# Kernel optimization log

Measured on AMD Instinct MI355X. Metric: run time of the kernel, lower is better.

The kernel has to match this reference:

```python
import jax, jax.numpy as jnp
import numpy as np

B, S, C, V, LAT, NL = 256, 512, 256, 32, 256, 7
DILS = [1, 2, 4, 8, 16, 32, 64]
EPS = 1e-5


def setup_inputs() -> dict:
    key = jax.random.key(0)
    ks = jax.random.split(key, 24)
    s = 0.05
    inp = {
        "x": jax.random.randint(ks[0], (B, S), 0, V, dtype=jnp.int64 if jax.config.read("jax_enable_x64") else jnp.int32),
        "z": jax.random.normal(ks[1], (B, LAT), dtype=jnp.float32),
        "emb": jax.random.normal(ks[2], (V, C), dtype=jnp.float32) * s,
        "latent_W": jax.random.normal(ks[3], (LAT, C), dtype=jnp.float32) * s,
        "latent_b": jnp.zeros((C,), jnp.float32),
        "ln1_g": jnp.ones((NL, C), jnp.float32),
        "ln1_b": jnp.zeros((NL, C), jnp.float32),
        "w1": jax.random.normal(ks[4], (NL, C, C), jnp.float32) * s,
        "b1": jnp.zeros((NL, C), jnp.float32),
        "ln2_g": jnp.ones((NL, C), jnp.float32),
        "ln2_b": jnp.zeros((NL, C), jnp.float32),
        "wd": jax.random.normal(ks[5], (NL, 2, C, C), jnp.float32) * s,  # tap 0 = x[t-d], tap 1 = x[t]
        "bd": jnp.zeros((NL, C), jnp.float32),
        "ln3_g": jnp.ones((NL, C), jnp.float32),
        "ln3_b": jnp.zeros((NL, C), jnp.float32),
        "we": jax.random.normal(ks[6], (NL, C, C), jnp.float32) * s,
        "be": jnp.zeros((NL, C), jnp.float32),
        "wg": jax.random.normal(ks[7], (NL, C, C), jnp.float32) * s,
        "bg": jnp.zeros((NL, C), jnp.float32),
        "out_W": jax.random.normal(ks[8], (C, V), jnp.float32) * s,
        "out_b": jnp.zeros((V,), jnp.float32),
    }
    return inp


def _ln(h, g, b):
    mu = h.mean(-1, keepdims=True)
    var = jnp.mean((h - mu) ** 2, axis=-1, keepdims=True)
    return (h - mu) * jax.lax.rsqrt(var + EPS) * g + b


def _lrelu(h):
    return jnp.where(h >= 0, h, 0.01 * h)


def reference(x, z, emb, latent_W, latent_b, ln1_g, ln1_b, w1, b1,
              ln2_g, ln2_b, wd, bd, ln3_g, ln3_b, we, be, wg, bg,
              out_W, out_b):
    # channel-last layout [B, S, C] throughout (fuses away the torch transposes)
    h = emb[x] + (z @ latent_W + latent_b)[:, None, :]
    for i, d in enumerate(DILS):
        x_inp = h
        t = _lrelu(_ln(x_inp, ln1_g[i], ln1_b[i]))
        t = t @ w1[i] + b1[i]
        t = _lrelu(_ln(t, ln2_g[i], ln2_b[i]))
        # causal dilated conv, kernel=2: out[t] = W0*x[t-d] + W1*x[t]
        t_shift = jnp.pad(t, ((0, 0), (d, 0), (0, 0)))[:, :t.shape[1], :]
        t = t_shift @ wd[i, 0] + t @ wd[i, 1] + bd[i]
        t = _lrelu(_ln(t, ln3_g[i], ln3_b[i]))
        gated = (t @ we[i] + be[i]) * jax.nn.sigmoid(t @ wg[i] + bg[i])
        h = gated + x_inp
    logits = h @ out_W + out_b                      # [B, S, V]
    lp = jax.nn.log_softmax(logits, axis=-1)
    # gather log-prob of next token: lp[:, :-1, :] at x[:, 1:]
    return jnp.take_along_axis(lp[:, :-1, :], x[:, 1:, None], axis=2)[..., 0]
```

## Files before the change

### kernel.cpp

```cpp
#include <hip/hip_runtime.h>

typedef unsigned short u16;
typedef unsigned int   u32;
typedef __attribute__((ext_vector_type(8))) short short8;
typedef __attribute__((ext_vector_type(4))) float f32x4;

struct __align__(8) u16x4 { u16 x, y, z, w; };

#define NL 7
#define M_DIM 131072

__device__ __forceinline__ float b2f(u16 u) {
  union { float f; u32 i; } c; c.i = ((u32)u) << 16; return c.f;
}
__device__ __forceinline__ u16 f2b(float f) {
  union { float f; u32 i; } c; c.f = f;
  u32 r = c.i + 0x7FFFu + ((c.i >> 16) & 1u);
  return (u16)(r >> 16);
}
__device__ __forceinline__ float wave_sum(float v) {
  #pragma unroll
  for (int off = 1; off < 64; off <<= 1) v += __shfl_xor(v, off);
  return v;
}
__device__ __forceinline__ void gload16(const void* g, void* l) {
  __builtin_amdgcn_global_load_lds((const __attribute__((address_space(1))) void*)g,
                                   (__attribute__((address_space(3))) void*)l, 16, 0, 0);
}


__global__ __launch_bounds__(256) void conv_w1_k(const float* __restrict__ w1, u16* __restrict__ wT) {
  int idx = blockIdx.x * 256 + threadIdx.x;
  int i = idx >> 16, rem = idx & 65535;
  int n = rem >> 8, k = rem & 255;
  wT[idx] = f2b(w1[(i << 16) + (k << 8) + n]);
}

__global__ __launch_bounds__(256) void conv_wd_k(const float* __restrict__ wd, u16* __restrict__ wT) {
  int idx = blockIdx.x * 256 + threadIdx.x;
  int i = idx / 131072, rem = idx & 131071;
  int n = rem >> 9, k2 = rem & 511;
  int tap = k2 >> 8, k = k2 & 255;
  wT[idx] = f2b(wd[(((i * 2 + tap) << 8) + k) * 256 + n]);
}

__global__ __launch_bounds__(256) void conv_weg_k(const float* __restrict__ we, const float* __restrict__ wg,
                                                  u16* __restrict__ wT) {
  int idx = blockIdx.x * 256 + threadIdx.x;
  int i = idx / 131072, rem = idx & 131071;
  int src = rem >> 16, n = (rem >> 8) & 255, k = rem & 255;
  const float* W = src ? wg : we;
  wT[idx] = f2b(W[((i << 8) + k) * 256 + n]);
}

__global__ __launch_bounds__(256) void conv_wo_k(const float* __restrict__ outW, u16* __restrict__ wTo) {
  int idx = blockIdx.x * 256 + threadIdx.x;
  int v = idx >> 8, k = idx & 255;
  wTo[idx] = f2b(outW[k * 32 + v]);
}


__global__ __launch_bounds__(256) void zlat_k(const float* __restrict__ z, const float* __restrict__ W,
                                              const float* __restrict__ bias, float* __restrict__ zlat) {
  int b = blockIdx.x, c = threadIdx.x;
  float acc = bias[c];
  for (int l = 0; l < 256; ++l) acc += z[b * 256 + l] * W[l * 256 + c];
  zlat[b * 256 + c] = acc;
}


__device__ __forceinline__ void ln_lrelu4(float v0, float v1, float v2, float v3,
                                          const float* __restrict__ g, const float* __restrict__ b,
                                          int c, u16x4* out) {
  float s = wave_sum(v0 + v1 + v2 + v3);
  float q = wave_sum(v0 * v0 + v1 * v1 + v2 * v2 + v3 * v3);
  float mu = s * 0.00390625f;
  float var = q * 0.00390625f - mu * mu;
  float rs = rsqrtf(var + 1e-5f);
  float4 gv = *(const float4*)&g[c];
  float4 bv = *(const float4*)&b[c];
  float y0 = (v0 - mu) * rs * gv.x + bv.x; y0 = y0 >= 0.f ? y0 : 0.01f * y0;
  float y1 = (v1 - mu) * rs * gv.y + bv.y; y1 = y1 >= 0.f ? y1 : 0.01f * y1;
  float y2 = (v2 - mu) * rs * gv.z + bv.z; y2 = y2 >= 0.f ? y2 : 0.01f * y2;
  float y3 = (v3 - mu) * rs * gv.w + bv.w; y3 = y3 >= 0.f ? y3 : 0.01f * y3;
  out->x = f2b(y0); out->y = f2b(y1); out->z = f2b(y2); out->w = f2b(y3);
}


__global__ __launch_bounds__(256) void embed_ln_k(const int* __restrict__ x, const float* __restrict__ emb,
                                                  const float* __restrict__ zlat,
                                                  const float* __restrict__ g, const float* __restrict__ b,
                                                  u16* __restrict__ h, u16* __restrict__ tOut) {
  int wave = threadIdx.x >> 6, lane = threadIdx.x & 63;
  int r = blockIdx.x * 4 + wave;
  int c = lane * 4;
  int tok = x[r];
  int bi = r >> 9;
  float4 ev = *(const float4*)&emb[tok * 256 + c];
  float4 zv = *(const float4*)&zlat[bi * 256 + c];
  float v0 = ev.x + zv.x, v1 = ev.y + zv.y, v2 = ev.z + zv.z, v3 = ev.w + zv.w;
  u16x4 hb; hb.x = f2b(v0); hb.y = f2b(v1); hb.z = f2b(v2); hb.w = f2b(v3);
  *(u16x4*)&h[(long)r * 256 + c] = hb;
  u16x4 ov;
  ln_lrelu4(v0, v1, v2, v3, g, b, c, &ov);
  *(u16x4*)&tOut[(long)r * 256 + c] = ov;
}


__global__ __launch_bounds__(256) void gemm_ln_k(
    const u16* __restrict__ A, const u16* __restrict__ WT, int Ktot, int dil,
    const float* __restrict__ bias, const float* __restrict__ g, const float* __restrict__ b,
    u16* __restrict__ Out)
{
  __shared__ u16 lA[64 * 32];
  __shared__ u16 lB[256 * 32];
  __shared__ float pS[64][4], pQ[64][4];
  __shared__ float muA[64], rsA[64];
  const int tid = threadIdx.x;
  const int lane = tid & 63;
  const int wv = tid >> 6;
  const int wc = wv * 64;
  const int m0 = blockIdx.x * 64;
  const int rA = tid >> 2;
  const int cSw = ((((tid & 3) - ((tid >> 3) & 3)) & 3)) * 8;
  const int mm = m0 + rA;
  const int s1 = mm & 511;
  const bool fixBlk = (dil > 0) && ((m0 & 511) < dil);

  const int lr = lane & 15;
  const int quad = lane >> 4;
  const int sw = ((quad + ((lr >> 1) & 3)) & 3) * 8;

  f32x4 acc[4][4];
  #pragma unroll
  for (int i = 0; i < 4; ++i)
    #pragma unroll
    for (int j = 0; j < 4; ++j) {
      acc[i][j][0] = 0.f; acc[i][j][1] = 0.f; acc[i][j][2] = 0.f; acc[i][j][3] = 0.f;
    }

  const int nkt = Ktot >> 5;
  for (int kt = 0; kt < nkt; ++kt) {
    const int kk = (kt & 7) * 32;
    int r = mm;
    if (dil > 0 && kt < 8) r = (s1 >= dil) ? (mm - dil) : mm;
    gload16(A + (long)r * 256 + kk + cSw, &lA[tid * 8]);
    const u16* bSrc = WT + (long)rA * Ktot + kt * 32 + cSw;
    #pragma unroll
    for (int j = 0; j < 4; ++j)
      gload16(bSrc + (long)(64 * j) * Ktot, &lB[tid * 8 + j * 2048]);
    __syncthreads();

    if (fixBlk && kt < 8) {
      if (rA < dil) {
        uint4 zz; zz.x = 0; zz.y = 0; zz.z = 0; zz.w = 0;
        *(uint4*)&lA[rA * 32 + (tid & 3) * 8] = zz;
      }
      __syncthreads();
    }

    short8 af[4], bfr[4];
    #pragma unroll
    for (int mt = 0; mt < 4; ++mt)
      af[mt] = *(const short8*)&lA[(mt * 16 + lr) * 32 + sw];
    #pragma unroll
    for (int nt = 0; nt < 4; ++nt)
      bfr[nt] = *(const short8*)&lB[(wc + nt * 16 + lr) * 32 + sw];
    #pragma unroll
    for (int mt = 0; mt < 4; ++mt)
      #pragma unroll
      for (int nt = 0; nt < 4; ++nt)
        acc[mt][nt] = __builtin_amdgcn_mfma_f32_16x16x32_bf16(af[mt], bfr[nt], acc[mt][nt], 0, 0, 0);
    __syncthreads();
  }

  float biasv[4], gv[4], bv[4];
  #pragma unroll
  for (int nt = 0; nt < 4; ++nt) {
    int n = wc + nt * 16 + lr;
    biasv[nt] = bias[n]; gv[nt] = g[n]; bv[nt] = b[n];
  }
  #pragma unroll
  for (int mt = 0; mt < 4; ++mt)
    #pragma unroll
    for (int r = 0; r < 4; ++r) {
      float s = 0.f, q = 0.f;
      #pragma unroll
      for (int nt = 0; nt < 4; ++nt) {
        float v = acc[mt][nt][r] + biasv[nt];
        acc[mt][nt][r] = v;
        s += v; q += v * v;
      }
      #pragma unroll
      for (int off = 1; off < 16; off <<= 1) {
        s += __shfl_xor(s, off); q += __shfl_xor(q, off);
      }
      if (lr == 0) { pS[mt * 16 + quad * 4 + r][wv] = s; pQ[mt * 16 + quad * 4 + r][wv] = q; }
    }
  __syncthreads();
  if (tid < 64) {
    float S = pS[tid][0] + pS[tid][1] + pS[tid][2] + pS[tid][3];
    float Q = pQ[tid][0] + pQ[tid][1] + pQ[tid][2] + pQ[tid][3];
    float mu = S * 0.00390625f;
    float var = Q * 0.00390625f - mu * mu;
    muA[tid] = mu; rsA[tid] = rsqrtf(var + 1e-5f);
  }
  __syncthreads();
  #pragma unroll
  for (int mt = 0; mt < 4; ++mt)
    #pragma unroll
    for (int r = 0; r < 4; ++r) {
      int row = mt * 16 + quad * 4 + r;
      float mu = muA[row], rs = rsA[row];
      #pragma unroll
      for (int nt = 0; nt < 4; ++nt) {
        float y = (acc[mt][nt][r] - mu) * rs * gv[nt] + bv[nt];
        y = y >= 0.f ? y : 0.01f * y;
        Out[(long)(m0 + row) * 256 + wc + nt * 16 + lr] = f2b(y);
      }
    }
}


__global__ __launch_bounds__(256, 2) void gemm_gate_ln_k(
    const u16* __restrict__ P, const u16* __restrict__ WTe, const u16* __restrict__ WTg,
    const float* __restrict__ be, const float* __restrict__ bg,
    const float* __restrict__ g, const float* __restrict__ b,
    u16* __restrict__ h, u16* __restrict__ tOut, int doLN)
{
  __shared__ u16 lA[64 * 32];
  __shared__ u16 lBe[256 * 32];
  __shared__ u16 lBg[256 * 32];
  __shared__ float pS[64][4], pQ[64][4];
  __shared__ float muA[64], rsA[64];
  const int tid = threadIdx.x;
  const int lane = tid & 63;
  const int wv = tid >> 6;
  const int wc = wv * 64;
  const int m0 = blockIdx.x * 64;
  const int rA = tid >> 2;
  const int cSw = ((((tid & 3) - ((tid >> 3) & 3)) & 3)) * 8;

  const int lr = lane & 15;
  const int quad = lane >> 4;
  const int sw = ((quad + ((lr >> 1) & 3)) & 3) * 8;

  f32x4 accE[4][4], accG[4][4];
  #pragma unroll
  for (int i = 0; i < 4; ++i)
    #pragma unroll
    for (int j = 0; j < 4; ++j) {
      accE[i][j][0] = 0.f; accE[i][j][1] = 0.f; accE[i][j][2] = 0.f; accE[i][j][3] = 0.f;
      accG[i][j][0] = 0.f; accG[i][j][1] = 0.f; accG[i][j][2] = 0.f; accG[i][j][3] = 0.f;
    }

  for (int kt = 0; kt < 8; ++kt) {
    const int kk = kt * 32;
    gload16(P + (long)(m0 + rA) * 256 + kk + cSw, &lA[tid * 8]);
    const long bofs = (long)rA * 256 + kk + cSw;
    #pragma unroll
    for (int j = 0; j < 4; ++j) {
      gload16(WTe + bofs + (long)(64 * j) * 256, &lBe[tid * 8 + j * 2048]);
      gload16(WTg + bofs + (long)(64 * j) * 256, &lBg[tid * 8 + j * 2048]);
    }
    __syncthreads();

    short8 af[4], bfe[4], bfg[4];
    #pragma unroll
    for (int mt = 0; mt < 4; ++mt)
      af[mt] = *(const short8*)&lA[(mt * 16 + lr) * 32 + sw];
    #pragma unroll
    for (int nt = 0; nt < 4; ++nt) {
      bfe[nt] = *(const short8*)&lBe[(wc + nt * 16 + lr) * 32 + sw];
      bfg[nt] = *(const short8*)&lBg[(wc + nt * 16 + lr) * 32 + sw];
    }
    #pragma unroll
    for (int mt = 0; mt < 4; ++mt)
      #pragma unroll
      for (int nt = 0; nt < 4; ++nt) {
        accE[mt][nt] = __builtin_amdgcn_mfma_f32_16x16x32_bf16(af[mt], bfe[nt], accE[mt][nt], 0, 0, 0);
        accG[mt][nt] = __builtin_amdgcn_mfma_f32_16x16x32_bf16(af[mt], bfg[nt], accG[mt][nt], 0, 0, 0);
      }
    __syncthreads();
  }

  float bev[4], bgv[4];
  #pragma unroll
  for (int nt = 0; nt < 4; ++nt) {
    int n = wc + nt * 16 + lr;
    bev[nt] = be[n]; bgv[nt] = bg[n];
  }
  #pragma unroll
  for (int mt = 0; mt < 4; ++mt)
    #pragma unroll
    for (int r = 0; r < 4; ++r) {
      int row = mt * 16 + quad * 4 + r;
      long off = (long)(m0 + row) * 256;
      float s = 0.f, q = 0.f;
      #pragma unroll
      for (int nt = 0; nt < 4; ++nt) {
        int n = wc + nt * 16 + lr;
        float e = accE[mt][nt][r] + bev[nt];
        float gg = accG[mt][nt][r] + bgv[nt];
        float hv = b2f(h[off + n]);
        float hn = e * (1.f / (1.f + expf(-gg))) + hv;
        h[off + n] = f2b(hn);
        accE[mt][nt][r] = hn;
        s += hn; q += hn * hn;
      }
      #pragma unroll
      for (int off2 = 1; off2 < 16; off2 <<= 1) {
        s += __shfl_xor(s, off2); q += __shfl_xor(q, off2);
      }
      if (lr == 0) { pS[row][wv] = s; pQ[row][wv] = q; }
    }
  __syncthreads();
  if (tid < 64) {
    float S = pS[tid][0] + pS[tid][1] + pS[tid][2] + pS[tid][3];
    float Q = pQ[tid][0] + pQ[tid][1] + pQ[tid][2] + pQ[tid][3];
    float mu = S * 0.00390625f;
    float var = Q * 0.00390625f - mu * mu;
    muA[tid] = mu; rsA[tid] = rsqrtf(var + 1e-5f);
  }
  __syncthreads();
  if (doLN) {
    float gv[4], bv[4];
    #pragma unroll
    for (int nt = 0; nt < 4; ++nt) {
      int n = wc + nt * 16 + lr;
      gv[nt] = g[n]; bv[nt] = b[n];
    }
    #pragma unroll
    for (int mt = 0; mt < 4; ++mt)
      #pragma unroll
      for (int r = 0; r < 4; ++r) {
        int row = mt * 16 + quad * 4 + r;
        float mu = muA[row], rs = rsA[row];
        #pragma unroll
        for (int nt = 0; nt < 4; ++nt) {
          float y = (accE[mt][nt][r] - mu) * rs * gv[nt] + bv[nt];
          y = y >= 0.f ? y : 0.01f * y;
          tOut[(long)(m0 + row) * 256 + wc + nt * 16 + lr] = f2b(y);
        }
      }
  }
}


__global__ __launch_bounds__(256) void final_k(const u16* __restrict__ h, const u16* __restrict__ WTo,
                                               const float* __restrict__ outb, const int* __restrict__ x,
                                               float* __restrict__ out) {
  __shared__ u16 lW[32 * 264];
  const int tid = threadIdx.x;
  const int lane = tid & 63;
  const int wv = tid >> 6;
  const int mBase = blockIdx.x * 256 + wv * 64;

  #pragma unroll
  for (int j = 0; j < 4; ++j) {
    int chunk = tid + 256 * j;
    int v = chunk >> 5, k8 = chunk & 31;
    uint4 w4 = *(const uint4*)(WTo + v * 256 + k8 * 8);
    *(uint4*)&lW[v * 264 + k8 * 8] = w4;
  }
  __syncthreads();

  const int lq = (lane >> 4) * 8;
  const int lr = lane & 15;
  const int quad = lane >> 4;

  f32x4 acc[4][2];
  #pragma unroll
  for (int mt = 0; mt < 4; ++mt) {
    acc[mt][0][0] = 0.f; acc[mt][0][1] = 0.f; acc[mt][0][2] = 0.f; acc[mt][0][3] = 0.f;
    acc[mt][1][0] = 0.f; acc[mt][1][1] = 0.f; acc[mt][1][2] = 0.f; acc[mt][1][3] = 0.f;
  }

  for (int kt = 0; kt < 8; ++kt) {
    short8 bf0 = *(const short8*)&lW[lr * 264 + kt * 32 + lq];
    short8 bf1 = *(const short8*)&lW[(16 + lr) * 264 + kt * 32 + lq];
    #pragma unroll
    for (int mt = 0; mt < 4; ++mt) {
      short8 af = *(const short8*)(h + (long)(mBase + mt * 16 + lr) * 256 + kt * 32 + lq);
      acc[mt][0] = __builtin_amdgcn_mfma_f32_16x16x32_bf16(af, bf0, acc[mt][0], 0, 0, 0);
      acc[mt][1] = __builtin_amdgcn_mfma_f32_16x16x32_bf16(af, bf1, acc[mt][1], 0, 0, 0);
    }
  }

  float ob0 = outb[lr], ob1 = outb[16 + lr];
  #pragma unroll
  for (int mt = 0; mt < 4; ++mt)
    #pragma unroll
    for (int r = 0; r < 4; ++r) {
      int row = mBase + mt * 16 + quad * 4 + r;
      float lo = acc[mt][0][r] + ob0;
      float hi = acc[mt][1][r] + ob1;
      float mx = fmaxf(lo, hi);
      #pragma unroll
      for (int o = 1; o < 16; o <<= 1) mx = fmaxf(mx, __shfl_xor(mx, o));
      float se = expf(lo - mx) + expf(hi - mx);
      #pragma unroll
      for (int o = 1; o < 16; o <<= 1) se += __shfl_xor(se, o);
      int s = row & 511;
      int xa = (s == 511) ? row : (row + 1);
      int tok = x[xa];
      float lg = (tok < 16) ? lo : hi;
      float lp = lg - mx - logf(se);
      if (s != 511 && lr == (tok & 15))
        out[(row >> 9) * 511 + s] = lp;
    }
}


extern "C" void kernel_launch(void* const* d_in, const int* in_sizes, int n_in,
                              void* d_out, int out_size, void* d_ws, size_t ws_size,
                              hipStream_t stream) {
  const int*   x    = (const int*)d_in[0];
  const float* z    = (const float*)d_in[1];
  const float* emb  = (const float*)d_in[2];
  const float* latW = (const float*)d_in[3];
  const float* latb = (const float*)d_in[4];
  const float* ln1g = (const float*)d_in[5];
  const float* ln1b = (const float*)d_in[6];
  const float* w1   = (const float*)d_in[7];
  const float* b1   = (const float*)d_in[8];
  const float* ln2g = (const float*)d_in[9];
  const float* ln2b = (const float*)d_in[10];
  const float* wd   = (const float*)d_in[11];
  const float* bd   = (const float*)d_in[12];
  const float* ln3g = (const float*)d_in[13];
  const float* ln3b = (const float*)d_in[14];
  const float* we   = (const float*)d_in[15];
  const float* be   = (const float*)d_in[16];
  const float* wg   = (const float*)d_in[17];
  const float* bg   = (const float*)d_in[18];
  const float* outW = (const float*)d_in[19];
  const float* outb = (const float*)d_in[20];

  char* ws = (char*)d_ws;
  u16*   h    = (u16*)(ws + 0);
  u16*   bufA = (u16*)(ws + 67108864);
  u16*   bufB = (u16*)(ws + 134217728);
  float* zlat = (float*)(ws + 201326592);
  u16*   wT1  = (u16*)(ws + 201588736);
  u16*   wTd  = (u16*)(ws + 202506240);
  u16*   wTeg = (u16*)(ws + 204341248);
  u16*   wTo  = (u16*)(ws + 206176256);

  conv_w1_k <<<1792, 256, 0, stream>>>(w1, wT1);
  conv_wd_k <<<3584, 256, 0, stream>>>(wd, wTd);
  conv_weg_k<<<3584, 256, 0, stream>>>(we, wg, wTeg);
  conv_wo_k <<<32, 256, 0, stream>>>(outW, wTo);
  zlat_k    <<<256, 256, 0, stream>>>(z, latW, latb, zlat);
  embed_ln_k<<<M_DIM / 4, 256, 0, stream>>>(x, emb, zlat, ln1g, ln1b, h, bufA);

  u16* X = bufA;
  u16* Y = bufB;
  for (int i = 0; i < NL; ++i) {
    int d = 1 << i;
    int doLN = (i < NL - 1) ? 1 : 0;
    int ni = doLN ? (i + 1) : i;
    gemm_ln_k<<<M_DIM / 64, 256, 0, stream>>>(
        X, wT1 + i * 65536, 256, 0, b1 + i * 256, ln2g + i * 256, ln2b + i * 256, Y);
    gemm_ln_k<<<M_DIM / 64, 256, 0, stream>>>(
        Y, wTd + i * 131072, 512, d, bd + i * 256, ln3g + i * 256, ln3b + i * 256, X);
    gemm_gate_ln_k<<<M_DIM / 64, 256, 0, stream>>>(
        X, wTeg + i * 131072, wTeg + i * 131072 + 65536, be + i * 256, bg + i * 256,
        ln1g + ni * 256, ln1b + ni * 256, h, Y, doLN);
    u16* tmp = X; X = Y; Y = tmp;
  }

  final_k<<<M_DIM / 256, 256, 0, stream>>>(h, wTo, outb, x, (float*)d_out);
}
```

Baseline: 1.667 ms.

## Enlarge GEMM row tiles to 128 and split gate GEMM across more waves

The row tile of both GEMM+LayerNorm kernels doubles to 128 rows, with 8 waves (gemm_ln) or 16 waves (gate kernel) laid out as an M×N wave grid, so each weight tile loaded into LDS is reused by twice as many rows. In the gate kernel each wave now computes only the E or only the G accumulator. Sigmoid results pass between waves through an LDS exchange buffer stored as bf16, which halves per-wave register pressure but adds a barrier and rounds the gate to bf16. The dilation zero-fix condition is changed to apply only to blocks at sequence start.

```diff
diff --git a/kernel.cpp b/kernel.cpp
--- a/kernel.cpp
+++ b/kernel.cpp
@@ -107,26 +107,26 @@
 }
 
 
-__global__ __launch_bounds__(256) void gemm_ln_k(
+__global__ __launch_bounds__(512, 4) void gemm_ln_k(
     const u16* __restrict__ A, const u16* __restrict__ WT, int Ktot, int dil,
     const float* __restrict__ bias, const float* __restrict__ g, const float* __restrict__ b,
     u16* __restrict__ Out)
 {
-  __shared__ u16 lA[64 * 32];
+  __shared__ u16 lA[128 * 32];
   __shared__ u16 lB[256 * 32];
-  __shared__ float pS[64][4], pQ[64][4];
-  __shared__ float muA[64], rsA[64];
+  __shared__ float pS[128][4], pQ[128][4];
+  __shared__ float muA[128], rsA[128];
   const int tid = threadIdx.x;
   const int lane = tid & 63;
   const int wv = tid >> 6;
-  const int wc = wv * 64;
-  const int m0 = blockIdx.x * 64;
+  const int mw = wv >> 2;
+  const int nw = wv & 3;
+  const int m0 = blockIdx.x * 128;
   const int rA = tid >> 2;
   const int cSw = ((((tid & 3) - ((tid >> 3) & 3)) & 3)) * 8;
   const int mm = m0 + rA;
   const int s1 = mm & 511;
-  const bool fixBlk = (dil > 0) && ((m0 & 511) < dil);
-
+  const bool fixBlk = (dil > 0) && ((m0 & 511) == 0);
   const int lr = lane & 15;
   const int quad = lane >> 4;
   const int sw = ((quad + ((lr >> 1) & 3)) & 3) * 8;
@@ -145,10 +145,9 @@
     int r = mm;
     if (dil > 0 && kt < 8) r = (s1 >= dil) ? (mm - dil) : mm;
     gload16(A + (long)r * 256 + kk + cSw, &lA[tid * 8]);
-    const u16* bSrc = WT + (long)rA * Ktot + kt * 32 + cSw;
-    #pragma unroll
-    for (int j = 0; j < 4; ++j)
-      gload16(bSrc + (long)(64 * j) * Ktot, &lB[tid * 8 + j * 2048]);
+    const u16* bSrc = WT + kt * 32 + cSw;
+    gload16(bSrc + (long)rA * Ktot,         &lB[tid * 8]);
+    gload16(bSrc + (long)(rA + 128) * Ktot, &lB[tid * 8 + 4096]);
     __syncthreads();
 
     if (fixBlk && kt < 8) {
@@ -162,10 +161,10 @@
     short8 af[4], bfr[4];
     #pragma unroll
     for (int mt = 0; mt < 4; ++mt)
-      af[mt] = *(const short8*)&lA[(mt * 16 + lr) * 32 + sw];
+      af[mt] = *(const short8*)&lA[(mw * 64 + mt * 16 + lr) * 32 + sw];
     #pragma unroll
     for (int nt = 0; nt < 4; ++nt)
-      bfr[nt] = *(const short8*)&lB[(wc + nt * 16 + lr) * 32 + sw];
+      bfr[nt] = *(const short8*)&lB[(nw * 64 + nt * 16 + lr) * 32 + sw];
     #pragma unroll
     for (int mt = 0; mt < 4; ++mt)
       #pragma unroll
@@ -177,7 +176,7 @@
   float biasv[4], gv[4], bv[4];
   #pragma unroll
   for (int nt = 0; nt < 4; ++nt) {
-    int n = wc + nt * 16 + lr;
+    int n = nw * 64 + nt * 16 + lr;
     biasv[nt] = bias[n]; gv[nt] = g[n]; bv[nt] = b[n];
   }
   #pragma unroll
@@ -195,10 +194,13 @@
       for (int off = 1; off < 16; off <<= 1) {
         s += __shfl_xor(s, off); q += __shfl_xor(q, off);
       }
-      if (lr == 0) { pS[mt * 16 + quad * 4 + r][wv] = s; pQ[mt * 16 + quad * 4 + r][wv] = q; }
-    }
-  __syncthreads();
-  if (tid < 64) {
+      if (lr == 0) {
+        int row = mw * 64 + mt * 16 + quad * 4 + r;
+        pS[row][nw] = s; pQ[row][nw] = q;
+      }
+    }
+  __syncthreads();
+  if (tid < 128) {
     float S = pS[tid][0] + pS[tid][1] + pS[tid][2] + pS[tid][3];
     float Q = pQ[tid][0] + pQ[tid][1] + pQ[tid][2] + pQ[tid][3];
     float mu = S * 0.00390625f;
@@ -210,137 +212,152 @@
   for (int mt = 0; mt < 4; ++mt)
     #pragma unroll
     for (int r = 0; r < 4; ++r) {
-      int row = mt * 16 + quad * 4 + r;
+      int row = mw * 64 + mt * 16 + quad * 4 + r;
       float mu = muA[row], rs = rsA[row];
       #pragma unroll
       for (int nt = 0; nt < 4; ++nt) {
         float y = (acc[mt][nt][r] - mu) * rs * gv[nt] + bv[nt];
         y = y >= 0.f ? y : 0.01f * y;
-        Out[(long)(m0 + row) * 256 + wc + nt * 16 + lr] = f2b(y);
-      }
-    }
-}
-
-
-__global__ __launch_bounds__(256, 2) void gemm_gate_ln_k(
+        Out[(long)(m0 + row) * 256 + nw * 64 + nt * 16 + lr] = f2b(y);
+      }
+    }
+}
+
+
+__global__ __launch_bounds__(1024) void gemm_gate_ln_k(
     const u16* __restrict__ P, const u16* __restrict__ WTe, const u16* __restrict__ WTg,
     const float* __restrict__ be, const float* __restrict__ bg,
     const float* __restrict__ g, const float* __restrict__ b,
     u16* __restrict__ h, u16* __restrict__ tOut, int doLN)
 {
-  __shared__ u16 lA[64 * 32];
-  __shared__ u16 lBe[256 * 32];
-  __shared__ u16 lBg[256 * 32];
-  __shared__ float pS[64][4], pQ[64][4];
-  __shared__ float muA[64], rsA[64];
+  __shared__ __align__(16) char smem[72704];
+  u16* lA  = (u16*)smem;
+  u16* lBe = (u16*)(smem + 8192);
+  u16* lBg = (u16*)(smem + 24576);
+  u16* xch = (u16*)smem;
+  float* pS  = (float*)(smem + 67584);
+  float* pQ  = (float*)(smem + 67584 + 2048);
+  float* muA = (float*)(smem + 67584 + 4096);
+  float* rsA = (float*)(smem + 67584 + 4608);
   const int tid = threadIdx.x;
   const int lane = tid & 63;
   const int wv = tid >> 6;
-  const int wc = wv * 64;
-  const int m0 = blockIdx.x * 64;
+  const int eg = wv & 1;
+  const int mw = (wv >> 1) & 1;
+  const int nw = (wv >> 2) & 3;
+  const int m0 = blockIdx.x * 128;
   const int rA = tid >> 2;
   const int cSw = ((((tid & 3) - ((tid >> 3) & 3)) & 3)) * 8;
-
   const int lr = lane & 15;
   const int quad = lane >> 4;
   const int sw = ((quad + ((lr >> 1) & 3)) & 3) * 8;
 
-  f32x4 accE[4][4], accG[4][4];
+  f32x4 acc[4][4];
   #pragma unroll
   for (int i = 0; i < 4; ++i)
     #pragma unroll
     for (int j = 0; j < 4; ++j) {
-      accE[i][j][0] = 0.f; accE[i][j][1] = 0.f; accE[i][j][2] = 0.f; accE[i][j][3] = 0.f;
-      accG[i][j][0] = 0.f; accG[i][j][1] = 0.f; accG[i][j][2] = 0.f; accG[i][j][3] = 0.f;
-    }
+      acc[i][j][0] = 0.f; acc[i][j][1] = 0.f; acc[i][j][2] = 0.f; acc[i][j][3] = 0.f;
+    }
+
+  const u16* lBx = eg ? lBg : lBe;
 
   for (int kt = 0; kt < 8; ++kt) {
     const int kk = kt * 32;
-    gload16(P + (long)(m0 + rA) * 256 + kk + cSw, &lA[tid * 8]);
-    const long bofs = (long)rA * 256 + kk + cSw;
-    #pragma unroll
-    for (int j = 0; j < 4; ++j) {
-      gload16(WTe + bofs + (long)(64 * j) * 256, &lBe[tid * 8 + j * 2048]);
-      gload16(WTg + bofs + (long)(64 * j) * 256, &lBg[tid * 8 + j * 2048]);
-    }
+    if (tid < 512)
+      gload16(P + (long)(m0 + rA) * 256 + kk + cSw, &lA[tid * 8]);
+    gload16(WTe + (long)rA * 256 + kk + cSw, &lBe[tid * 8]);
+    gload16(WTg + (long)rA * 256 + kk + cSw, &lBg[tid * 8]);
     __syncthreads();
 
-    short8 af[4], bfe[4], bfg[4];
-    #pragma unroll
-    for (int mt = 0; mt < 4; ++mt)
-      af[mt] = *(const short8*)&lA[(mt * 16 + lr) * 32 + sw];
-    #pragma unroll
-    for (int nt = 0; nt < 4; ++nt) {
-      bfe[nt] = *(const short8*)&lBe[(wc + nt * 16 + lr) * 32 + sw];
-      bfg[nt] = *(const short8*)&lBg[(wc + nt * 16 + lr) * 32 + sw];
-    }
-    #pragma unroll
-    for (int mt = 0; mt < 4; ++mt)
-      #pragma unroll
-      for (int nt = 0; nt < 4; ++nt) {
-        accE[mt][nt] = __builtin_amdgcn_mfma_f32_16x16x32_bf16(af[mt], bfe[nt], accE[mt][nt], 0, 0, 0);
-        accG[mt][nt] = __builtin_amdgcn_mfma_f32_16x16x32_bf16(af[mt], bfg[nt], accG[mt][nt], 0, 0, 0);
-      }
+    short8 af[4], bf[4];
+    #pragma unroll
+    for (int mt = 0; mt < 4; ++mt)
+      af[mt] = *(const short8*)&lA[((mw * 64 + mt * 16 + lr) & 127) * 32 + sw];
+    #pragma unroll
+    for (int nt = 0; nt < 4; ++nt)
+      bf[nt] = *(const short8*)&lBx[(nw * 64 + nt * 16 + lr) * 32 + sw];
+    #pragma unroll
+    for (int mt = 0; mt < 4; ++mt)
+      #pragma unroll
+      for (int nt = 0; nt < 4; ++nt)
+        acc[mt][nt] = __builtin_amdgcn_mfma_f32_16x16x32_bf16(af[mt], bf[nt], acc[mt][nt], 0, 0, 0);
     __syncthreads();
   }
 
-  float bev[4], bgv[4];
+  float bxv[4];
   #pragma unroll
   for (int nt = 0; nt < 4; ++nt) {
-    int n = wc + nt * 16 + lr;
-    bev[nt] = be[n]; bgv[nt] = bg[n];
-  }
-  #pragma unroll
-  for (int mt = 0; mt < 4; ++mt)
-    #pragma unroll
-    for (int r = 0; r < 4; ++r) {
-      int row = mt * 16 + quad * 4 + r;
-      long off = (long)(m0 + row) * 256;
-      float s = 0.f, q = 0.f;
-      #pragma unroll
-      for (int nt = 0; nt < 4; ++nt) {
-        int n = wc + nt * 16 + lr;
-        float e = accE[mt][nt][r] + bev[nt];
-        float gg = accG[mt][nt][r] + bgv[nt];
-        float hv = b2f(h[off + n]);
-        float hn = e * (1.f / (1.f + expf(-gg))) + hv;
-        h[off + n] = f2b(hn);
-        accE[mt][nt][r] = hn;
-        s += hn; q += hn * hn;
-      }
-      #pragma unroll
-      for (int off2 = 1; off2 < 16; off2 <<= 1) {
-        s += __shfl_xor(s, off2); q += __shfl_xor(q, off2);
-      }
-      if (lr == 0) { pS[row][wv] = s; pQ[row][wv] = q; }
-    }
-  __syncthreads();
-  if (tid < 64) {
-    float S = pS[tid][0] + pS[tid][1] + pS[tid][2] + pS[tid][3];
-    float Q = pQ[tid][0] + pQ[tid][1] + pQ[tid][2] + pQ[tid][3];
+    int n = nw * 64 + nt * 16 + lr;
+    bxv[nt] = eg ? bg[n] : be[n];
+  }
+  if (eg) {
+    #pragma unroll
+    for (int mt = 0; mt < 4; ++mt)
+      #pragma unroll
+      for (int r = 0; r < 4; ++r) {
+        int row = mw * 64 + mt * 16 + quad * 4 + r;
+        #pragma unroll
+        for (int nt = 0; nt < 4; ++nt) {
+          int n = nw * 64 + nt * 16 + lr;
+          float gg = acc[mt][nt][r] + bxv[nt];
+          xch[row * 264 + n] = f2b(1.f / (1.f + expf(-gg)));
+        }
+      }
+  }
+  __syncthreads();
+  if (!eg) {
+    #pragma unroll
+    for (int mt = 0; mt < 4; ++mt)
+      #pragma unroll
+      for (int r = 0; r < 4; ++r) {
+        int row = mw * 64 + mt * 16 + quad * 4 + r;
+        long off = (long)(m0 + row) * 256;
+        float s = 0.f, q = 0.f;
+        #pragma unroll
+        for (int nt = 0; nt < 4; ++nt) {
+          int n = nw * 64 + nt * 16 + lr;
+          float e = acc[mt][nt][r] + bxv[nt];
+          float sg = b2f(xch[row * 264 + n]);
+          float hn = e * sg + b2f(h[off + n]);
+          h[off + n] = f2b(hn);
+          acc[mt][nt][r] = hn;
+          s += hn; q += hn * hn;
+        }
+        #pragma unroll
+        for (int o = 1; o < 16; o <<= 1) {
+          s += __shfl_xor(s, o); q += __shfl_xor(q, o);
+        }
+        if (lr == 0) { pS[row * 4 + nw] = s; pQ[row * 4 + nw] = q; }
+      }
+  }
+  __syncthreads();
+  if (tid < 128) {
+    float S = pS[tid * 4] + pS[tid * 4 + 1] + pS[tid * 4 + 2] + pS[tid * 4 + 3];
+    float Q = pQ[tid * 4] + pQ[tid * 4 + 1] + pQ[tid * 4 + 2] + pQ[tid * 4 + 3];
     float mu = S * 0.00390625f;
     float var = Q * 0.00390625f - mu * mu;
     muA[tid] = mu; rsA[tid] = rsqrtf(var + 1e-5f);
   }
   __syncthreads();
-  if (doLN) {
+  if (doLN && !eg) {
     float gv[4], bv[4];
     #pragma unroll
     for (int nt = 0; nt < 4; ++nt) {
-      int n = wc + nt * 16 + lr;
+      int n = nw * 64 + nt * 16 + lr;
       gv[nt] = g[n]; bv[nt] = b[n];
     }
     #pragma unroll
     for (int mt = 0; mt < 4; ++mt)
       #pragma unroll
       for (int r = 0; r < 4; ++r) {
-        int row = mt * 16 + quad * 4 + r;
+        int row = mw * 64 + mt * 16 + quad * 4 + r;
         float mu = muA[row], rs = rsA[row];
         #pragma unroll
         for (int nt = 0; nt < 4; ++nt) {
-          float y = (accE[mt][nt][r] - mu) * rs * gv[nt] + bv[nt];
+          float y = (acc[mt][nt][r] - mu) * rs * gv[nt] + bv[nt];
           y = y >= 0.f ? y : 0.01f * y;
-          tOut[(long)(m0 + row) * 256 + wc + nt * 16 + lr] = f2b(y);
+          tOut[(long)(m0 + row) * 256 + nw * 64 + nt * 16 + lr] = f2b(y);
         }
       }
   }
@@ -460,11 +477,11 @@
     int d = 1 << i;
     int doLN = (i < NL - 1) ? 1 : 0;
     int ni = doLN ? (i + 1) : i;
-    gemm_ln_k<<<M_DIM / 64, 256, 0, stream>>>(
+    gemm_ln_k<<<M_DIM / 128, 512, 0, stream>>>(
         X, wT1 + i * 65536, 256, 0, b1 + i * 256, ln2g + i * 256, ln2b + i * 256, Y);
-    gemm_ln_k<<<M_DIM / 64, 256, 0, stream>>>(
+    gemm_ln_k<<<M_DIM / 128, 512, 0, stream>>>(
         Y, wTd + i * 131072, 512, d, bd + i * 256, ln3g + i * 256, ln3b + i * 256, X);
-    gemm_gate_ln_k<<<M_DIM / 64, 256, 0, stream>>>(
+    gemm_gate_ln_k<<<M_DIM / 128, 1024, 0, stream>>>(
         X, wTeg + i * 131072, wTeg + i * 131072 + 65536, be + i * 256, bg + i * 256,
         ln1g + ni * 256, ln1b + ni * 256, h, Y, doLN);
     u16* tmp = X; X = Y; Y = tmp;
```

Result: slower. 1.790 ms (+7.4%).
